# Performance work log

Measured on AMD Instinct MI355X. Metric: run time of the kernel, lower is better.

The kernel has to match this reference:

```python
import jax, jax.numpy as jnp
import numpy as np


def _fps(xyz, S):
    """Farthest point sampling over one cloud. xyz: [N,3] -> idx [S] (int32).
    Deterministic start at index 0 (torch_cluster.fps uses a random start; the
    algorithm is otherwise identical)."""
    d0 = jnp.sum((xyz - xyz[0]) ** 2, axis=-1)  # squared dist to first pick

    def step(mind, _):
        nxt = jnp.argmax(mind)                              # farthest from selected set
        d = jnp.sum((xyz - xyz[nxt]) ** 2, axis=-1)
        return jnp.minimum(mind, d), nxt.astype(jnp.int32)

    _, rest = jax.lax.scan(step, d0, None, length=S - 1)
    return jnp.concatenate([jnp.zeros((1,), jnp.int32), rest])


def _gather(points, idx):
    """points [B,N,C], idx [B,...] -> [B,...,C] (per-batch fancy gather)."""
    return jax.vmap(lambda p, i: p[i])(points, idx)


def setup_inputs() -> dict:
    key = jax.random.key(0)
    k1, k2 = jax.random.split(key)
    B, N, C = 8, 4096, 64
    channel_out = C + 3  # use_xyz=True
    return {
        "xyz": jax.random.normal(k1, (B, N, 3), dtype=jnp.float32),
        "points": jax.random.normal(k2, (B, N, C), dtype=jnp.float32),
        "affine_alpha": jnp.ones((1, 1, 1, channel_out), dtype=jnp.float32),
        "affine_beta": jnp.zeros((1, 1, 1, channel_out), dtype=jnp.float32),
        "groups": 1024,
        "kneighbors": 32,
    }


def reference(xyz, points, affine_alpha, affine_beta, groups, kneighbors):
    B, N, _ = xyz.shape
    S, K = groups, kneighbors

    # --- FPS sample S centroids per batch ---
    fps_idx = jax.vmap(lambda x: _fps(x, S))(xyz)              # [B,S]
    new_xyz = _gather(xyz, fps_idx)                            # [B,S,3]
    new_points = _gather(points, fps_idx)                      # [B,S,C]

    # --- KNN: K nearest input points for each centroid ---
    # squared distances [B,S,N] via ||q||^2 + ||x||^2 - 2 q.x
    d2 = (jnp.sum(new_xyz ** 2, -1)[..., None]
          + jnp.sum(xyz ** 2, -1)[:, None, :]
          - 2.0 * jnp.einsum("bsc,bnc->bsn", new_xyz, xyz))
    idx = jax.lax.top_k(-d2, K)[1]                             # [B,S,K]

    grouped_xyz = _gather(xyz, idx)                            # [B,S,K,3]
    grouped_points = _gather(points, idx)                      # [B,S,K,C]
    grouped_points = jnp.concatenate([grouped_points, grouped_xyz], axis=-1)  # use_xyz

    # --- per-group center normalize + global (per-batch) std, affine ---
    mean = jnp.mean(grouped_points, axis=2, keepdims=True)     # [B,S,1,C+3]
    centered = grouped_points - mean
    std = jnp.std(centered.reshape(B, -1), axis=-1, ddof=1)    # unbiased, like torch.std
    std = std[:, None, None, None]
    grouped_points = centered / (std + 1e-5)
    grouped_points = affine_alpha * grouped_points + affine_beta

    new_points_out = jnp.concatenate(
        [grouped_points,
         jnp.broadcast_to(new_points[:, :, None, :], (B, S, K, new_points.shape[-1]))],
        axis=-1)                                               # [B,S,K,2C+3]
    return new_xyz, new_points_out
```

## Files before the change

### kernel.cpp

```cpp
#include <hip/hip_runtime.h>
#include <math.h>

#define NPTS 4096
#define NS 1024
#define NK 32
#define NC 64
#define NCG 67
#define NCOUT 131
#define NB 8
#define GRID 512

typedef float v2f __attribute__((ext_vector_type(2)));
typedef unsigned long long ull;

__device__ __forceinline__ float wave_max_dpp(float v) {
  int x = __float_as_int(v);
#define DPP_STEP(ctrl)                                                        \
  {                                                                           \
    int t = __builtin_amdgcn_update_dpp(x, x, ctrl, 0xF, 0xF, false);         \
    x = __float_as_int(fmaxf(__int_as_float(x), __int_as_float(t)));          \
  }
  DPP_STEP(0x111)
  DPP_STEP(0x112)
  DPP_STEP(0x114)
  DPP_STEP(0x118)
  DPP_STEP(0x142)
  DPP_STEP(0x143)
#undef DPP_STEP
  return __int_as_float(__builtin_amdgcn_readlane(x, 63));
}

__device__ __forceinline__ void wave_argmin_dpp(float& v, int& i) {
#define ARG_STEP(ctrl)                                                         \
  {                                                                            \
    int tv = __builtin_amdgcn_update_dpp(__float_as_int(v), __float_as_int(v), \
                                         ctrl, 0xF, 0xF, false);               \
    int ti = __builtin_amdgcn_update_dpp(i, i, ctrl, 0xF, 0xF, false);         \
    float ov = __int_as_float(tv);                                             \
    bool t = (ov < v) || (ov == v && ti < i);                                  \
    v = t ? ov : v;                                                            \
    i = t ? ti : i;                                                            \
  }
  ARG_STEP(0x111) ARG_STEP(0x112) ARG_STEP(0x114)
  ARG_STEP(0x118) ARG_STEP(0x142) ARG_STEP(0x143)
#undef ARG_STEP
  v = __int_as_float(__builtin_amdgcn_readlane(__float_as_int(v), 63));
  i = __builtin_amdgcn_readlane(i, 63);
}

__device__ __forceinline__ void lds_barrier() {
  asm volatile("s_waitcnt lgkmcnt(0)" ::: "memory");
  __builtin_amdgcn_s_barrier();
  asm volatile("" ::: "memory");
}

__device__ __forceinline__ void unpack4(const float4* __restrict__ X4,
                                        float* px, float* py, float* pz) {
  float4 a = X4[0], c = X4[1], e = X4[2];
  px[0] = a.x; py[0] = a.y; pz[0] = a.z;
  px[1] = a.w; py[1] = c.x; pz[1] = c.y;
  px[2] = c.z; py[2] = c.w; pz[2] = e.x;
  px[3] = e.y; py[3] = e.z; pz[3] = e.w;
}

__device__ __forceinline__ void unpack16(const float4* __restrict__ X4,
                                         float* px, float* py, float* pz) {
#pragma unroll
  for (int g = 0; g < 4; ++g) unpack4(X4 + 3 * g, px + 4 * g, py + 4 * g, pz + 4 * g);
}

__global__ __launch_bounds__(256) void fused_kernel(const float* __restrict__ xyz,
                                                    const float* __restrict__ points,
                                                    float* __restrict__ newxyz,
                                                    int* __restrict__ fps_idx,
                                                    int* __restrict__ knn_idx,
                                                    float* __restrict__ mean_ws,
                                                    float* __restrict__ part_ws,
                                                    int* pick_idx) {
  __shared__ float4 coords4[NPTS];
  __shared__ int fps_lds[NS];
  __shared__ ull keys[2][4];
  __shared__ float pvv[2][4];
  __shared__ int pii[2][4];
  __shared__ int idx_lds[NK];
  __shared__ float red[256];

  const int tid = threadIdx.x;
  const int lane = tid & 63;
  const int wav = tid >> 6;
  const int bx = blockIdx.x;

  if (bx < NB) {
#pragma clang fp contract(off)
    __builtin_amdgcn_s_setprio(3);
    const int b = bx;
    const float* X = xyz + (size_t)b * NPTS * 3;
    const int base = tid * 16;
    float px[16], py[16], pz[16];
    unpack16((const float4*)(X + (size_t)base * 3), px, py, pz);
#pragma unroll
    for (int j = 0; j < 16; ++j) coords4[base + j] = make_float4(px[j], py[j], pz[j], 0.0f);
    v2f px2[8], py2[8], pz2[8], mind2[8];
#pragma unroll
    for (int q = 0; q < 8; ++q) {
      px2[q] = v2f{px[2 * q], px[2 * q + 1]};
      py2[q] = v2f{py[2 * q], py[2 * q + 1]};
      pz2[q] = v2f{pz[2 * q], pz[2 * q + 1]};
      mind2[q] = v2f{__builtin_inff(), __builtin_inff()};
    }
    float cx = X[0], cy = X[1], cz = X[2];
    int gi = 0;
    if (tid == 0) fps_lds[0] = 0;
    __syncthreads();

    for (int s = 1; s < NS; ++s) {
      v2f cxv = v2f{cx, cx}, cyv = v2f{cy, cy}, czv = v2f{cz, cz};
      v2f runmax = v2f{-1.0f, -1.0f};
#pragma unroll
      for (int q = 0; q < 8; ++q) {
        v2f dx = px2[q] - cxv;
        v2f dy = py2[q] - cyv;
        v2f dz = pz2[q] - czv;
        v2f d = ((dx * dx) + (dy * dy)) + (dz * dz);
        v2f m = __builtin_elementwise_min(mind2[q], d);
        mind2[q] = m;
        runmax = __builtin_elementwise_max(runmax, m);
      }
      float bv = fmaxf(runmax.x, runmax.y);
      int bj = 0;
#pragma unroll
      for (int q = 7; q >= 0; --q) {
        bj = (mind2[q].y == bv) ? 2 * q + 1 : bj;
        bj = (mind2[q].x == bv) ? 2 * q : bj;
      }
      float smax = wave_max_dpp(bv);
      ull lm = __ballot(bv == smax);
      int wl = (int)(__ffsll(lm) - 1);
      int bjw = __builtin_amdgcn_readlane(bj, wl);
      int gidx = ((wav << 6) + wl) * 16 + bjw;
      ull key = ((ull)__float_as_uint(smax) << 32) |
                (ull)(0xFFFFFFFFu - (unsigned)gidx);
      const int p = s & 1;
      if (lane == 0) keys[p][wav] = key;
      lds_barrier();
      ull k0 = keys[p][0], k1 = keys[p][1], k2 = keys[p][2], k3 = keys[p][3];
      ull ka = k0 > k1 ? k0 : k1;
      ull kb = k2 > k3 ? k2 : k3;
      ull km = ka > kb ? ka : kb;
      gi = (int)(0xFFFFFFFFu - (unsigned)(km & 0xFFFFFFFFull));
      float4 c4 = coords4[gi];
      if (tid == 0) {
        fps_lds[s] = gi;
        __hip_atomic_store(&pick_idx[b * NS + s], gi, __ATOMIC_RELAXED,
                           __HIP_MEMORY_SCOPE_AGENT);
      }
      cx = c4.x; cy = c4.y; cz = c4.z;
    }
    __syncthreads();
    for (int s = tid; s < NS; s += 256) {
      int g2 = fps_lds[s];
      float4 c4 = coords4[g2];
      fps_idx[b * NS + s] = g2;
      newxyz[(size_t)(b * NS + s) * 3 + 0] = c4.x;
      newxyz[(size_t)(b * NS + s) * 3 + 1] = c4.y;
      newxyz[(size_t)(b * NS + s) * 3 + 2] = c4.z;
    }
  } else {
    if (bx >= 256 && bx < 256 + NB) return;
    const int w = (bx < 256) ? (bx - NB) : (bx - NB - NB);
    const int nwork = GRID - 2 * NB;
    for (int q = w; q < NB * NS; q += nwork) {
      const int b = q & 7;
      const int s = q >> 3;
      const int bs = (b << 10) | s;
      int gi = 0;
      if (s != 0) {
        gi = __hip_atomic_load(&pick_idx[bs], __ATOMIC_RELAXED, __HIP_MEMORY_SCOPE_AGENT);
        while (gi == -1) {
          __builtin_amdgcn_s_sleep(16);
          gi = __hip_atomic_load(&pick_idx[bs], __ATOMIC_RELAXED, __HIP_MEMORY_SCOPE_AGENT);
        }
      }
      const float* X = xyz + (size_t)b * NPTS * 3;
      const float sx = X[gi * 3 + 0];
      const float sy = X[gi * 3 + 1];
      const float sz = X[gi * 3 + 2];
      const float snorm = __fadd_rn(__fadd_rn(__fmul_rn(sx, sx), __fmul_rn(sy, sy)),
                                    __fmul_rn(sz, sz));
      const int base = tid * 16;
      const float4* X4 = (const float4*)(X + (size_t)base * 3);
      float d2[16];
      float bv = __builtin_inff(); int bi = 0x7fffffff;
#pragma unroll
      for (int g4 = 0; g4 < 4; ++g4) {
        float qx[4], qy[4], qz[4];
        unpack4(X4 + 3 * g4, qx, qy, qz);
#pragma unroll
        for (int j = 0; j < 4; ++j) {
          const int jj = 4 * g4 + j;
          float nn = __fadd_rn(__fadd_rn(__fmul_rn(qx[j], qx[j]), __fmul_rn(qy[j], qy[j])),
                               __fmul_rn(qz[j], qz[j]));
          float dt = __fmaf_rn(sz, qz[j], __fmaf_rn(sy, qy[j], __fmul_rn(sx, qx[j])));
          float d = __fsub_rn(__fadd_rn(snorm, nn), __fmul_rn(2.0f, dt));
          d2[jj] = d;
          if (d < bv) { bv = d; bi = base + jj; }
        }
      }
      float wv = bv; int wi = bi;
      wave_argmin_dpp(wv, wi);
      for (int k = 0; k < NK; ++k) {
        const int p = k & 1;
        if ((tid & 63) == 0) { pvv[p][wav] = wv; pii[p][wav] = wi; }
        __syncthreads();
        float gv = pvv[p][0]; int g2 = pii[p][0];
#pragma unroll
        for (int ww = 1; ww < 4; ++ww) {
          float ov = pvv[p][ww]; int oi = pii[p][ww];
          bool t = (ov < gv) || (ov == gv && oi < g2);
          if (t) { gv = ov; g2 = oi; }
        }
        if (tid == 0) idx_lds[k] = g2;
        if ((g2 >> 10) == wav) {
          if ((g2 >> 4) == tid) {
            bv = __builtin_inff(); bi = 0x7fffffff;
#pragma unroll
            for (int j = 0; j < 16; ++j) {
              float d = d2[j];
              if (base + j == g2) { d = __builtin_inff(); d2[j] = d; }
              if (d < bv) { bv = d; bi = base + j; }
            }
          }
          wv = bv; wi = bi;
          wave_argmin_dpp(wv, wi);
        }
      }
      __syncthreads();
      if (tid < NK) knn_idx[(size_t)bs * NK + tid] = idx_lds[tid];
      float acc = 0.0f;
      if (tid < NCG) {
        const float* Pb = points + (size_t)b * NPTS * NC;
        const float* Xb = xyz + (size_t)b * NPTS * 3;
        float sum = 0.0f, sumsq = 0.0f;
#pragma unroll
        for (int k = 0; k < NK; ++k) {
          int row = idx_lds[k];
          float g = (tid < NC) ? Pb[(size_t)row * NC + tid] : Xb[(size_t)row * 3 + (tid - NC)];
          sum += g;
          sumsq = __fmaf_rn(g, g, sumsq);
        }
        float m = sum * (1.0f / 32.0f);
        mean_ws[(size_t)bs * NCG + tid] = m;
        acc = __fmaf_rn(-m, sum, sumsq);
      }
      red[tid] = acc;
      __syncthreads();
      for (int off = 128; off > 0; off >>= 1) {
        if (tid < off) red[tid] += red[tid + off];
        __syncthreads();
      }
      if (tid == 0) part_ws[bs] = red[0];
      __syncthreads();
    }
  }
}

__global__ __launch_bounds__(256) void scale_kernel(const float* __restrict__ part_ws,
                                                    float* __restrict__ scale_ws) {
  const int b = blockIdx.x;
  const int tid = threadIdx.x;
  __shared__ float red[256];
  const float* p = part_ws + (size_t)b * NS;
  float a = p[tid] + p[tid + 256] + p[tid + 512] + p[tid + 768];
  red[tid] = a;
  __syncthreads();
  for (int off = 128; off > 0; off >>= 1) {
    if (tid < off) red[tid] += red[tid + off];
    __syncthreads();
  }
  if (tid == 0) {
    float var = red[0] / 2195455.0f;
    scale_ws[b] = 1.0f / (sqrtf(var) + 1e-5f);
  }
}

__global__ __launch_bounds__(256) void out_kernel(const float* __restrict__ xyz,
                                                  const float* __restrict__ points,
                                                  const float* __restrict__ alpha,
                                                  const float* __restrict__ beta,
                                                  const int* __restrict__ fps_idx,
                                                  const int* __restrict__ knn_idx,
                                                  const float* __restrict__ mean_ws,
                                                  const float* __restrict__ scale_ws,
                                                  float* __restrict__ out2) {
  const int bs = blockIdx.x;
  const int b = bs >> 10;
  const int tid = threadIdx.x;
  __shared__ int idx[NK];
  __shared__ float mrow[NCG], al[NCG], be[NCG];
  __shared__ int fr_s;
  if (tid < NK) idx[tid] = knn_idx[(size_t)bs * NK + tid];
  if (tid < NCG) {
    mrow[tid] = mean_ws[(size_t)bs * NCG + tid];
    al[tid] = alpha[tid];
    be[tid] = beta[tid];
  }
  if (tid == 0) fr_s = fps_idx[bs];
  __syncthreads();
  const float scl = scale_ws[b];
  const int fr = fr_s;
  const float* Pb = points + (size_t)b * NPTS * NC;
  const float* Xb = xyz + (size_t)b * NPTS * 3;
  float* orow = out2 + (size_t)bs * NK * NCOUT;
  const float* Fr = Pb + (size_t)fr * NC;
  for (int e4 = tid; e4 < NK * NCOUT / 4; e4 += 256) {
    float4 v4;
    float* vp = &v4.x;
#pragma unroll
    for (int j = 0; j < 4; ++j) {
      int e = 4 * e4 + j;
      int k = e / NCOUT;
      int c = e - k * NCOUT;
      float v;
      if (c < NCG) {
        int row = idx[k];
        float gv = (c < NC) ? Pb[(size_t)row * NC + c] : Xb[(size_t)row * 3 + (c - NC)];
        v = (gv - mrow[c]) * scl * al[c] + be[c];
      } else {
        v = Fr[c - NCG];
      }
      vp[j] = v;
    }
    ((float4*)orow)[e4] = v4;
  }
}

extern "C" void kernel_launch(void* const* d_in, const int* in_sizes, int n_in,
                              void* d_out, int out_size, void* d_ws, size_t ws_size,
                              hipStream_t stream) {
  const float* xyz    = (const float*)d_in[0];
  const float* points = (const float*)d_in[1];
  const float* alpha  = (const float*)d_in[2];
  const float* beta   = (const float*)d_in[3];

  float* out = (float*)d_out;
  float* newxyz = out;
  float* out2 = out + (size_t)NB * NS * 3;

  char* ws = (char*)d_ws;
  int*   fps_idx  = (int*)(ws + 0);
  int*   knn_idx  = (int*)(ws + 32768);
  float* mean_ws  = (float*)(ws + 1081344);
  float* part_ws  = (float*)(ws + 3276800);
  float* scale_ws = (float*)(ws + 3309568);
  int*   pick_idx = (int*)(ws + 3309632);

  hipMemsetAsync(pick_idx, 0xFF, NB * NS * sizeof(int), stream);

  fused_kernel<<<GRID,    256, 0, stream>>>(xyz, points, newxyz, fps_idx, knn_idx,
                                            mean_ws, part_ws, pick_idx);
  scale_kernel<<<NB,      256, 0, stream>>>(part_ws, scale_ws);
  out_kernel  <<<NB * NS, 256, 0, stream>>>(xyz, points, alpha, beta, fps_idx, knn_idx,
                                            mean_ws, scale_ws, out2);
}
```

Baseline: 656.9 us.

## Batch FPS picks via candidate-set pruning with single-wave inner selection

Adds a fast path to farthest point sampling. It counts points whose min-distance exceeds a fraction of the current max. If at most 64 qualify, one wave runs several successive FPS picks over that small candidate set using DPP argmax, with no block barriers. The picks end once the max falls below the threshold, and all threads then apply the batched picked centers to their min-distances. This removes many per-step block-wide reductions and barriers, at the cost of counting overhead, a periodic retry schedule, and more branchy control flow.

```diff
diff --git a/kernel.cpp b/kernel.cpp
--- a/kernel.cpp
+++ b/kernel.cpp
@@ -9,6 +9,7 @@
 #define NCOUT 131
 #define NB 8
 #define GRID 512
+#define MAXCAND 64
 
 typedef float v2f __attribute__((ext_vector_type(2)));
 typedef unsigned long long ull;
@@ -48,6 +49,24 @@
   i = __builtin_amdgcn_readlane(i, 63);
 }
 
+__device__ __forceinline__ void wave_argmax_idx_dpp(float& v, int& i) {
+#define ARG_STEP(ctrl)                                                         \
+  {                                                                            \
+    int tv = __builtin_amdgcn_update_dpp(__float_as_int(v), __float_as_int(v), \
+                                         ctrl, 0xF, 0xF, false);               \
+    int ti = __builtin_amdgcn_update_dpp(i, i, ctrl, 0xF, 0xF, false);         \
+    float ov = __int_as_float(tv);                                             \
+    bool t = (ov > v) || (ov == v && ti < i);                                  \
+    v = t ? ov : v;                                                            \
+    i = t ? ti : i;                                                            \
+  }
+  ARG_STEP(0x111) ARG_STEP(0x112) ARG_STEP(0x114)
+  ARG_STEP(0x118) ARG_STEP(0x142) ARG_STEP(0x143)
+#undef ARG_STEP
+  v = __int_as_float(__builtin_amdgcn_readlane(__float_as_int(v), 63));
+  i = __builtin_amdgcn_readlane(i, 63);
+}
+
 __device__ __forceinline__ void lds_barrier() {
   asm volatile("s_waitcnt lgkmcnt(0)" ::: "memory");
   __builtin_amdgcn_s_barrier();
@@ -79,7 +98,13 @@
                                                     int* pick_idx) {
   __shared__ float4 coords4[NPTS];
   __shared__ int fps_lds[NS];
-  __shared__ ull keys[2][4];
+  __shared__ ull skey[2][4];
+  __shared__ ull ckey[4];
+  __shared__ float4 candv[MAXCAND];
+  __shared__ int candi[MAXCAND];
+  __shared__ float4 pend[MAXCAND];
+  __shared__ int lcnt;
+  __shared__ int ctrl_pc;
   __shared__ float pvv[2][4];
   __shared__ int pii[2][4];
   __shared__ int idx_lds[NK];
@@ -113,7 +138,11 @@
     if (tid == 0) fps_lds[0] = 0;
     __syncthreads();
 
-    for (int s = 1; s < NS; ++s) {
+    int s = 1;
+    int slowskip = 63;
+
+    while (s < NS) {
+      if (tid == 0) lcnt = 0;
       v2f cxv = v2f{cx, cx}, cyv = v2f{cy, cy}, czv = v2f{cz, cz};
       v2f runmax = v2f{-1.0f, -1.0f};
 #pragma unroll
@@ -133,37 +162,151 @@
         bj = (mind2[q].y == bv) ? 2 * q + 1 : bj;
         bj = (mind2[q].x == bv) ? 2 * q : bj;
       }
-      float smax = wave_max_dpp(bv);
-      ull lm = __ballot(bv == smax);
+      float smaxw = wave_max_dpp(bv);
+      ull lm = __ballot(bv == smaxw);
       int wl = (int)(__ffsll(lm) - 1);
       int bjw = __builtin_amdgcn_readlane(bj, wl);
       int gidx = ((wav << 6) + wl) * 16 + bjw;
-      ull key = ((ull)__float_as_uint(smax) << 32) |
+      ull key = ((ull)__float_as_uint(smaxw) << 32) |
                 (ull)(0xFFFFFFFFu - (unsigned)gidx);
-      const int p = s & 1;
-      if (lane == 0) keys[p][wav] = key;
+      if (lane == 0) skey[s & 1][wav] = key;
       lds_barrier();
-      ull k0 = keys[p][0], k1 = keys[p][1], k2 = keys[p][2], k3 = keys[p][3];
+      ull k0 = skey[s & 1][0], k1 = skey[s & 1][1];
+      ull k2 = skey[s & 1][2], k3 = skey[s & 1][3];
       ull ka = k0 > k1 ? k0 : k1;
       ull kb = k2 > k3 ? k2 : k3;
       ull km = ka > kb ? ka : kb;
-      gi = (int)(0xFFFFFFFFu - (unsigned)(km & 0xFFFFFFFFull));
-      float4 c4 = coords4[gi];
-      if (tid == 0) {
-        fps_lds[s] = gi;
-        __hip_atomic_store(&pick_idx[b * NS + s], gi, __ATOMIC_RELAXED,
-                           __HIP_MEMORY_SCOPE_AGENT);
-      }
-      cx = c4.x; cy = c4.y; cz = c4.z;
+      float gm = __uint_as_float((unsigned)(km >> 32));
+      int gig = (int)(0xFFFFFFFFu - (unsigned)(km & 0xFFFFFFFFull));
+
+      bool fast = false;
+      float T = 0.0f;
+      if (slowskip == 0) {
+        float T1 = 0.5f * gm, T2 = 0.75f * gm, T3 = 0.875f * gm;
+        int c1 = 0, c2 = 0, c3 = 0;
+#pragma unroll
+        for (int q = 0; q < 8; ++q) {
+          float mx = mind2[q].x, my = mind2[q].y;
+          c1 += (mx > T1) + (my > T1);
+          c2 += (mx > T2) + (my > T2);
+          c3 += (mx > T3) + (my > T3);
+        }
+        for (int off = 1; off < 64; off <<= 1) {
+          c1 += __shfl_xor(c1, off);
+          c2 += __shfl_xor(c2, off);
+          c3 += __shfl_xor(c3, off);
+        }
+        if (lane == 0)
+          ckey[wav] = ((ull)(unsigned)c1 << 42) | ((ull)(unsigned)c2 << 21) |
+                      (ull)(unsigned)c3;
+        lds_barrier();
+        ull cs = ckey[0] + ckey[1] + ckey[2] + ckey[3];
+        int cnt1 = (int)(cs >> 42);
+        int cnt2 = (int)((cs >> 21) & 0x1FFFFF);
+        int cnt3 = (int)(cs & 0x1FFFFF);
+        if (gm > 0.0f) {
+          if (cnt1 <= MAXCAND)      { fast = true; T = T1; }
+          else if (cnt2 <= MAXCAND) { fast = true; T = T2; }
+          else if (cnt3 <= MAXCAND) { fast = true; T = T3; }
+        }
+        if (!fast) slowskip = 7;
+      } else {
+        --slowskip;
+      }
+
+      if (!fast) {
+        gi = gig;
+        float4 c4 = coords4[gi];
+        if (tid == 0) {
+          fps_lds[s] = gi;
+          __hip_atomic_store(&pick_idx[b * NS + s], gi, __ATOMIC_RELAXED,
+                             __HIP_MEMORY_SCOPE_AGENT);
+        }
+        cx = c4.x; cy = c4.y; cz = c4.z;
+        ++s;
+        continue;
+      }
+
+#pragma unroll
+      for (int q = 0; q < 8; ++q) {
+        if (mind2[q].x > T) {
+          int pos = atomicAdd(&lcnt, 1);
+          candv[pos] = make_float4(mind2[q].x, px2[q].x, py2[q].x, pz2[q].x);
+          candi[pos] = base + 2 * q;
+        }
+        if (mind2[q].y > T) {
+          int pos = atomicAdd(&lcnt, 1);
+          candv[pos] = make_float4(mind2[q].y, px2[q].y, py2[q].y, pz2[q].y);
+          candi[pos] = base + 2 * q + 1;
+        }
+      }
+      lds_barrier();
+
+      if (wav == 0) {
+        int cnt = lcnt;
+        float v_, cxx = 0.f, cyy = 0.f, czz = 0.f;
+        int i_;
+        if (lane < cnt) {
+          float4 cv = candv[lane];
+          v_ = cv.x; cxx = cv.y; cyy = cv.z; czz = cv.w;
+          i_ = candi[lane];
+        } else {
+          v_ = -__builtin_inff();
+          i_ = 0x7fffffff;
+        }
+        float lx = cx, ly = cy, lz = cz;
+        int pc = 0, scur = s;
+        for (;;) {
+          if (scur >= NS) break;
+          float dx = cxx - lx, dy = cyy - ly, dz = czz - lz;
+          float d = ((dx * dx) + (dy * dy)) + (dz * dz);
+          v_ = fminf(v_, d);
+          float v2 = v_; int i2 = i_;
+          wave_argmax_idx_dpp(v2, i2);
+          if (!(v2 > T)) break;
+          ull wm = __ballot(v_ == v2 && i_ == i2);
+          int wl2 = (int)(__ffsll(wm) - 1);
+          lx = __int_as_float(__builtin_amdgcn_readlane(__float_as_int(cxx), wl2));
+          ly = __int_as_float(__builtin_amdgcn_readlane(__float_as_int(cyy), wl2));
+          lz = __int_as_float(__builtin_amdgcn_readlane(__float_as_int(czz), wl2));
+          if (lane == wl2) v_ = -__builtin_inff();
+          if (lane == 0) {
+            fps_lds[scur] = i2;
+            __hip_atomic_store(&pick_idx[b * NS + scur], i2, __ATOMIC_RELAXED,
+                               __HIP_MEMORY_SCOPE_AGENT);
+            pend[pc] = make_float4(lx, ly, lz, 0.0f);
+          }
+          ++pc; ++scur;
+        }
+        if (lane == 0) ctrl_pc = pc;
+      }
+      lds_barrier();
+
+      int pc = ctrl_pc;
+      for (int pp = 0; pp < pc; ++pp) {
+        float4 c4 = pend[pp];
+        v2f pxv = v2f{c4.x, c4.x}, pyv = v2f{c4.y, c4.y}, pzv = v2f{c4.z, c4.z};
+#pragma unroll
+        for (int q = 0; q < 8; ++q) {
+          v2f dx = px2[q] - pxv;
+          v2f dy = py2[q] - pyv;
+          v2f dz = pz2[q] - pzv;
+          v2f d = ((dx * dx) + (dy * dy)) + (dz * dz);
+          mind2[q] = __builtin_elementwise_min(mind2[q], d);
+        }
+        if (pp == pc - 1) { cx = c4.x; cy = c4.y; cz = c4.z; }
+      }
+      s += pc;
     }
+
     __syncthreads();
-    for (int s = tid; s < NS; s += 256) {
-      int g2 = fps_lds[s];
+    for (int s2 = tid; s2 < NS; s2 += 256) {
+      int g2 = fps_lds[s2];
       float4 c4 = coords4[g2];
-      fps_idx[b * NS + s] = g2;
-      newxyz[(size_t)(b * NS + s) * 3 + 0] = c4.x;
-      newxyz[(size_t)(b * NS + s) * 3 + 1] = c4.y;
-      newxyz[(size_t)(b * NS + s) * 3 + 2] = c4.z;
+      fps_idx[b * NS + s2] = g2;
+      newxyz[(size_t)(b * NS + s2) * 3 + 0] = c4.x;
+      newxyz[(size_t)(b * NS + s2) * 3 + 1] = c4.y;
+      newxyz[(size_t)(b * NS + s2) * 3 + 2] = c4.z;
     }
   } else {
     if (bx >= 256 && bx < 256 + NB) return;
```

New measurement: 869.6 us. 32.4% more time.
